# Performance work log

Hardware: AMD Instinct MI355X
Metric: run time of the kernel (lower is better)

## Reference

```python
import jax, jax.numpy as jnp
import numpy as np

D_MODEL = 1024
NUM_HEADS = 16
HEAD_DIM = D_MODEL // NUM_HEADS
BATCH, SEQ = 2, 2048


def setup_inputs() -> dict:
    key = jax.random.key(0)
    ks = jax.random.split(key, 11)
    s = 1.0 / np.sqrt(D_MODEL)
    inp = {
        "query": jax.random.normal(ks[0], (BATCH, SEQ, D_MODEL), jnp.float32),
        "key": jax.random.normal(ks[1], (BATCH, SEQ, D_MODEL), jnp.float32),
        "value": jax.random.normal(ks[2], (BATCH, SEQ, D_MODEL), jnp.float32),
        "q_w": jax.random.uniform(ks[3], (D_MODEL, D_MODEL), jnp.float32, -s, s),
        "q_b": jax.random.uniform(ks[4], (D_MODEL,), jnp.float32, -s, s),
        "k_w": jax.random.uniform(ks[5], (D_MODEL, D_MODEL), jnp.float32, -s, s),
        "k_b": jax.random.uniform(ks[6], (D_MODEL,), jnp.float32, -s, s),
        "v_w": jax.random.uniform(ks[7], (D_MODEL, D_MODEL), jnp.float32, -s, s),
        "v_b": jax.random.uniform(ks[8], (D_MODEL,), jnp.float32, -s, s),
        "o_w": jax.random.uniform(ks[9], (D_MODEL, D_MODEL), jnp.float32, -s, s),
        "o_b": jax.random.uniform(ks[10], (D_MODEL,), jnp.float32, -s, s),
    }
    return inp


def reference(query, key, value, q_w, q_b, k_w, k_b, v_w, v_b, o_w, o_b):
    B = query.shape[0]
    # linear projections (torch Linear: x @ W^T + b)
    q = query @ q_w.T + q_b
    k = key @ k_w.T + k_b
    v = value @ v_w.T + v_b
    # split heads: [B, S, D] -> [B, H, S, Hd]
    def split(x):
        return x.reshape(B, -1, NUM_HEADS, HEAD_DIM).transpose(0, 2, 1, 3)
    q, k, v = split(q), split(k), split(v)
    scores = jnp.einsum("bhqd,bhkd->bhqk", q, k) / np.sqrt(HEAD_DIM).astype(np.float32)
    attn = jax.nn.softmax(scores, axis=-1)
    out = jnp.einsum("bhqk,bhkd->bhqd", attn, v)  # [B,H,S,Hd]
    merged = out.transpose(0, 2, 1, 3).reshape(B, -1, D_MODEL)
    return merged @ o_w.T + o_b
```

## Files before the change

### kernel.cpp

```cpp
#include <hip/hip_runtime.h>
#include <hip/hip_bf16.h>

typedef unsigned short u16;
typedef unsigned int u32;
typedef __attribute__((ext_vector_type(8))) short short8;
typedef __attribute__((ext_vector_type(4))) short s16x4;
typedef __attribute__((ext_vector_type(4))) float f32x4;
typedef __attribute__((ext_vector_type(4))) u32 u32v4;

__device__ __forceinline__ u16 f2bf(float f) {
    u32 u = __float_as_uint(f);
    return (u16)((u + 0x7FFFu + ((u >> 16) & 1u)) >> 16);
}
__device__ __forceinline__ u32 pack2bf(float a, float b) {
    __hip_bfloat162 h = __float22bfloat162_rn(float2{a, b});
    return *reinterpret_cast<u32*>(&h);
}

#if __has_builtin(__builtin_amdgcn_exp2f)
#define EXP2(x) __builtin_amdgcn_exp2f(x)
#else
#define EXP2(x) exp2f(x)
#endif

__device__ __forceinline__ void gload16(const void* g, void* s) {
    __builtin_amdgcn_global_load_lds(
        (const __attribute__((address_space(1))) void*)g,
        (__attribute__((address_space(3))) void*)s, 16, 0, 0);
}

__global__ __launch_bounds__(256) void cast_all_kernel(
    const float* __restrict__ s0, const float* __restrict__ s1, const float* __restrict__ s2,
    const float* __restrict__ s3, const float* __restrict__ s4, const float* __restrict__ s5,
    const float* __restrict__ s6,
    u16* __restrict__ d0, u16* __restrict__ d1, u16* __restrict__ d2,
    u16* __restrict__ d3, u16* __restrict__ d4, u16* __restrict__ d5,
    u16* __restrict__ d6, int nBig, int nSmall)
{
    const int y = blockIdx.y;
    const float* s = y == 0 ? s0 : (y == 1 ? s1 : (y == 2 ? s2 : (y == 3 ? s3 : (y == 4 ? s4 : (y == 5 ? s5 : s6)))));
    u16* d = y == 0 ? d0 : (y == 1 ? d1 : (y == 2 ? d2 : (y == 3 ? d3 : (y == 4 ? d4 : (y == 5 ? d5 : d6)))));
    const int n = (y < 3) ? nBig : nSmall;
    int i = (blockIdx.x * 256 + threadIdx.x) * 4;
    const int stride = gridDim.x * 256 * 4;
    for (; i < n; i += stride) {
        float4 v = *(const float4*)(s + i);
        uint2 t;
        t.x = pack2bf(v.x, v.y);
        t.y = pack2bf(v.z, v.w);
        *(uint2*)(d + i) = t;
    }
}

__global__ __launch_bounds__(256) void qkv_gemm(
    const u16* __restrict__ Xq, const u16* __restrict__ Xk, const u16* __restrict__ Xv,
    const u16* __restrict__ Wq, const u16* __restrict__ Wk, const u16* __restrict__ Wv,
    const float* __restrict__ qb, const float* __restrict__ kb, const float* __restrict__ vb,
    u16* __restrict__ Qo, u16* __restrict__ Ko, u16* __restrict__ Vo)
{
    constexpr int N = 1024, K = 1024;
    __shared__ __align__(16) u16 Asm[2][4096];
    __shared__ __align__(16) u16 Bsm[2][4096];
    const int z = blockIdx.z;
    const u16* A = z == 0 ? Xq : (z == 1 ? Xk : Xv);
    const u16* W = z == 0 ? Wq : (z == 1 ? Wk : Wv);
    const float* bias = z == 0 ? qb : (z == 1 ? kb : vb);

    const int tid = threadIdx.x;
    const int wid = tid >> 6;
    const int lane = tid & 63;
    const int r15 = lane & 15, g = lane >> 4;
    const int fb = blockIdx.y * 8 + blockIdx.x;
    const int lsw = (fb & 7) * 32 + (fb >> 3);
    const int m0 = (lsw >> 3) * 128, n0 = (lsw & 7) * 128;
    const int wr = wid >> 1, wc = wid & 1;

    f32x4 acc[4][4];
#pragma unroll
    for (int i = 0; i < 4; ++i)
#pragma unroll
        for (int j = 0; j < 4; ++j) acc[i][j] = (f32x4){0.f, 0.f, 0.f, 0.f};

    const int idx0 = tid, idx1 = tid + 256;
    const size_t aoff0 = (size_t)(m0 + (idx0 >> 2)) * K + (idx0 & 3) * 8;
    const size_t aoff1 = (size_t)(m0 + (idx1 >> 2)) * K + (idx1 & 3) * 8;
    const size_t boff0 = (size_t)(n0 + (idx0 >> 2)) * K + (idx0 & 3) * 8;
    const size_t boff1 = (size_t)(n0 + (idx1 >> 2)) * K + (idx1 & 3) * 8;

    auto STAGE = [&](int buf, int kt) {
        gload16(A + aoff0 + kt, &Asm[buf][wid * 512]);
        gload16(A + aoff1 + kt, &Asm[buf][2048 + wid * 512]);
        gload16(W + boff0 + kt, &Bsm[buf][wid * 512]);
        gload16(W + boff1 + kt, &Bsm[buf][2048 + wid * 512]);
    };

    STAGE(0, 0);
    __syncthreads();
    for (int t = 0; t < 32; ++t) {
        const int buf = t & 1;
        if (t < 31) STAGE(buf ^ 1, (t + 1) * 32);
        short8 af[4], bfr[4];
#pragma unroll
        for (int i = 0; i < 4; ++i) {
            af[i]  = *(const short8*)(&Asm[buf][0] + (wr * 64 + i * 16 + r15) * 32 + g * 8);
            bfr[i] = *(const short8*)(&Bsm[buf][0] + (wc * 64 + i * 16 + r15) * 32 + g * 8);
        }
#pragma unroll
        for (int i = 0; i < 4; ++i)
#pragma unroll
            for (int j = 0; j < 4; ++j)
                acc[i][j] = __builtin_amdgcn_mfma_f32_16x16x32_bf16(af[i], bfr[j], acc[i][j], 0, 0, 0);
        __syncthreads();
    }

    const float scale = (z == 0) ? 0.125f * 1.4426950408889634f : 1.0f;
    u16* ob = z == 0 ? Qo : (z == 1 ? Ko : Vo);
#pragma unroll
    for (int i = 0; i < 4; ++i) {
        const int mbase = m0 + wr * 64 + i * 16 + g * 4;
#pragma unroll
        for (int j = 0; j < 4; ++j) {
            const int n = n0 + wc * 64 + j * 16 + r15;
            const float bb = bias[n];
            if (z < 2) {
#pragma unroll
                for (int r = 0; r < 4; ++r)
                    ob[(size_t)(mbase + r) * N + n] = f2bf((acc[i][j][r] + bb) * scale);
            } else {
                const int b_ = mbase >> 11, s_ = mbase & 2047;
                const int blk = (s_ >> 2) & 7;
                const int pb = ((blk & 3) << 1) | (blk >> 2);
                const int s_new = (s_ & ~31) | (pb << 2);
                s16x4 pk;
#pragma unroll
                for (int r = 0; r < 4; ++r) pk[r] = (short)f2bf(acc[i][j][r] + bb);
                *(s16x4*)(ob + ((size_t)b_ << 21) + (size_t)n * 2048 + s_new) = pk;
            }
        }
    }
}

__global__ __launch_bounds__(256) void o_gemm(
    const u16* __restrict__ A, const u16* __restrict__ W,
    const float* __restrict__ bias, float* __restrict__ outp)
{
    constexpr int N = 1024, K = 1024;
    __shared__ __align__(16) u16 Asm[2][4096];
    __shared__ __align__(16) u16 Bsm[2][4096];
    const int tid = threadIdx.x;
    const int wid = tid >> 6;
    const int lane = tid & 63;
    const int r15 = lane & 15, g = lane >> 4;
    const int fb = blockIdx.y * 8 + blockIdx.x;
    const int lsw = (fb & 7) * 32 + (fb >> 3);
    const int m0 = (lsw >> 3) * 128, n0 = (lsw & 7) * 128;
    const int wr = wid >> 1, wc = wid & 1;

    f32x4 acc[4][4];
#pragma unroll
    for (int i = 0; i < 4; ++i)
#pragma unroll
        for (int j = 0; j < 4; ++j) acc[i][j] = (f32x4){0.f, 0.f, 0.f, 0.f};

    const int idx0 = tid, idx1 = tid + 256;
    const size_t aoff0 = (size_t)(m0 + (idx0 >> 2)) * K + (idx0 & 3) * 8;
    const size_t aoff1 = (size_t)(m0 + (idx1 >> 2)) * K + (idx1 & 3) * 8;
    const size_t boff0 = (size_t)(n0 + (idx0 >> 2)) * K + (idx0 & 3) * 8;
    const size_t boff1 = (size_t)(n0 + (idx1 >> 2)) * K + (idx1 & 3) * 8;

    auto STAGE = [&](int buf, int kt) {
        gload16(A + aoff0 + kt, &Asm[buf][wid * 512]);
        gload16(A + aoff1 + kt, &Asm[buf][2048 + wid * 512]);
        gload16(W + boff0 + kt, &Bsm[buf][wid * 512]);
        gload16(W + boff1 + kt, &Bsm[buf][2048 + wid * 512]);
    };

    STAGE(0, 0);
    __syncthreads();
    for (int t = 0; t < 32; ++t) {
        const int buf = t & 1;
        if (t < 31) STAGE(buf ^ 1, (t + 1) * 32);
        short8 af[4], bfr[4];
#pragma unroll
        for (int i = 0; i < 4; ++i) {
            af[i]  = *(const short8*)(&Asm[buf][0] + (wr * 64 + i * 16 + r15) * 32 + g * 8);
            bfr[i] = *(const short8*)(&Bsm[buf][0] + (wc * 64 + i * 16 + r15) * 32 + g * 8);
        }
#pragma unroll
        for (int i = 0; i < 4; ++i)
#pragma unroll
            for (int j = 0; j < 4; ++j)
                acc[i][j] = __builtin_amdgcn_mfma_f32_16x16x32_bf16(af[i], bfr[j], acc[i][j], 0, 0, 0);
        __syncthreads();
    }

#pragma unroll
    for (int i = 0; i < 4; ++i) {
        const int mbase = m0 + wr * 64 + i * 16 + g * 4;
#pragma unroll
        for (int j = 0; j < 4; ++j) {
            const int n = n0 + wc * 64 + j * 16 + r15;
            const float bb = bias[n];
#pragma unroll
            for (int r = 0; r < 4; ++r)
                outp[(size_t)(mbase + r) * N + n] = acc[i][j][r] + bb;
        }
    }
}

__global__ __launch_bounds__(256) void attn_kernel(
    const u16* __restrict__ Q, const u16* __restrict__ Kb,
    const u16* __restrict__ Vt, u16* __restrict__ Mo)
{
    __shared__ __align__(16) u16 Ksm[2][4096];
    __shared__ __align__(16) u16 Vsm[2][4096];
    const int tid = threadIdx.x;
    const int wid = tid >> 6, lane = tid & 63;
    const int r15 = lane & 15, g = lane >> 4;
    const int bid = blockIdx.x;
    const int l = (bid & 7) * 64 + (bid >> 3);
    const int bh = l >> 4;
    const int b = bh >> 4, h = bh & 15;
    const int q0 = (l & 15) * 128 + wid * 32;

    const u16* Qbase = Q + ((size_t)b * 2048 + q0) * 1024 + h * 64;
    short8 qf[2][2];
#pragma unroll
    for (int qt = 0; qt < 2; ++qt)
#pragma unroll
        for (int f = 0; f < 2; ++f)
            qf[qt][f] = *(const short8*)(Qbase + (size_t)(qt * 16 + r15) * 1024 + f * 32 + g * 8);

    const int p0 = tid, p1 = tid + 256;
    const int row0 = p0 >> 3, slot0 = (p0 & 7) ^ (row0 & 7);
    const int row1 = p1 >> 3, slot1 = (p1 & 7) ^ (row1 & 7);
    const u16* Ks0 = Kb + ((size_t)b * 2048 + row0) * 1024 + h * 64 + slot0 * 8;
    const u16* Ks1 = Kb + ((size_t)b * 2048 + row1) * 1024 + h * 64 + slot1 * 8;
    const u16* Vs0 = Vt + ((size_t)b << 21) + (size_t)(h * 64 + row0) * 2048 + slot0 * 8;
    const u16* Vs1 = Vt + ((size_t)b << 21) + (size_t)(h * 64 + row1) * 2048 + slot1 * 8;

    f32x4 acc[2][4];
#pragma unroll
    for (int qt = 0; qt < 2; ++qt)
#pragma unroll
        for (int d4 = 0; d4 < 4; ++d4) acc[qt][d4] = (f32x4){0.f, 0.f, 0.f, 0.f};
    float lsum[2] = {0.f, 0.f};

    auto STAGE = [&](int buf, int k0) {
        gload16(Ks0 + (size_t)k0 * 1024, &Ksm[buf][wid * 512]);
        gload16(Ks1 + (size_t)k0 * 1024, &Ksm[buf][2048 + wid * 512]);
        gload16(Vs0 + k0, &Vsm[buf][wid * 512]);
        gload16(Vs1 + k0, &Vsm[buf][2048 + wid * 512]);
    };

    STAGE(0, 0);
    __syncthreads();

    const int sA = r15 & 7;
    for (int t = 0; t < 32; ++t) {
        const int buf = t & 1;
        if (t < 31) STAGE(buf ^ 1, (t + 1) * 64);

        const u16* Kp = &Ksm[buf][0];
        const u16* Vp = &Vsm[buf][0];
        short8 kf[4][2];
#pragma unroll
        for (int kt = 0; kt < 4; ++kt)
#pragma unroll
            for (int f = 0; f < 2; ++f)
                kf[kt][f] = *(const short8*)(Kp + (kt * 16 + r15) * 64 + (((f * 4 + g) ^ sA) * 8));

        f32x4 st[2][4];
#pragma unroll
        for (int qt = 0; qt < 2; ++qt)
#pragma unroll
            for (int kt = 0; kt < 4; ++kt) {
                f32x4 zz = (f32x4){0.f, 0.f, 0.f, 0.f};
                zz = __builtin_amdgcn_mfma_f32_16x16x32_bf16(kf[kt][0], qf[qt][0], zz, 0, 0, 0);
                zz = __builtin_amdgcn_mfma_f32_16x16x32_bf16(kf[kt][1], qf[qt][1], zz, 0, 0, 0);
                st[qt][kt] = zz;
            }

        u32 pk[2][8];
#pragma unroll
        for (int qt = 0; qt < 2; ++qt) {
            float s = 0.f;
#pragma unroll
            for (int kt = 0; kt < 4; ++kt) {
                float e0 = EXP2(st[qt][kt][0]);
                float e1 = EXP2(st[qt][kt][1]);
                float e2 = EXP2(st[qt][kt][2]);
                float e3 = EXP2(st[qt][kt][3]);
                s += (e0 + e1) + (e2 + e3);
                pk[qt][kt * 2]     = pack2bf(e0, e1);
                pk[qt][kt * 2 + 1] = pack2bf(e2, e3);
            }
            lsum[qt] += s;
        }

#pragma unroll
        for (int d4 = 0; d4 < 4; ++d4) {
#pragma unroll
            for (int kk = 0; kk < 2; ++kk) {
                short8 vf = *(const short8*)(Vp + (d4 * 16 + r15) * 64 + (((kk * 4 + g) ^ sA) * 8));
                u32v4 b0 = {pk[0][kk * 4], pk[0][kk * 4 + 1], pk[0][kk * 4 + 2], pk[0][kk * 4 + 3]};
                u32v4 b1 = {pk[1][kk * 4], pk[1][kk * 4 + 1], pk[1][kk * 4 + 2], pk[1][kk * 4 + 3]};
                acc[0][d4] = __builtin_amdgcn_mfma_f32_16x16x32_bf16(vf, __builtin_bit_cast(short8, b0), acc[0][d4], 0, 0, 0);
                acc[1][d4] = __builtin_amdgcn_mfma_f32_16x16x32_bf16(vf, __builtin_bit_cast(short8, b1), acc[1][d4], 0, 0, 0);
            }
        }
        __syncthreads();
    }

#pragma unroll
    for (int qt = 0; qt < 2; ++qt) {
        float ls = lsum[qt];
        ls += __shfl_xor(ls, 16, 64);
        ls += __shfl_xor(ls, 32, 64);
        const float inv = 1.f / ls;
        const size_t orow = ((size_t)b * 2048 + q0 + qt * 16 + r15) * 1024 + h * 64;
#pragma unroll
        for (int d4 = 0; d4 < 4; ++d4) {
            uint2 o;
            o.x = pack2bf(acc[qt][d4][0] * inv, acc[qt][d4][1] * inv);
            o.y = pack2bf(acc[qt][d4][2] * inv, acc[qt][d4][3] * inv);
            *(uint2*)(Mo + orow + d4 * 16 + g * 4) = o;
        }
    }
}

extern "C" void kernel_launch(void* const* d_in, const int* in_sizes, int n_in,
                              void* d_out, int out_size, void* d_ws, size_t ws_size,
                              hipStream_t stream) {
    (void)in_sizes; (void)n_in; (void)out_size; (void)ws_size;
    const float* query = (const float*)d_in[0];
    const float* key   = (const float*)d_in[1];
    const float* value = (const float*)d_in[2];
    const float* q_w = (const float*)d_in[3];
    const float* q_b = (const float*)d_in[4];
    const float* k_w = (const float*)d_in[5];
    const float* k_b = (const float*)d_in[6];
    const float* v_w = (const float*)d_in[7];
    const float* v_b = (const float*)d_in[8];
    const float* o_w = (const float*)d_in[9];
    const float* o_b = (const float*)d_in[10];

    const size_t NE = (size_t)4096 * 1024;
    const size_t MW = (size_t)1024 * 1024;
    u16* w = (u16*)d_ws;
    u16* Xq = w;
    u16* Xk = Xq + NE;
    u16* Xv = Xk + NE;
    u16* Wq = Xv + NE;
    u16* Wk = Wq + MW;
    u16* Wv = Wk + MW;
    u16* Wo = Wv + MW;
    u16* Qb = Wo + MW;
    u16* Kb = Qb + NE;
    u16* Vt = Kb + NE;
    u16* Mo = Vt + NE;

    cast_all_kernel<<<dim3(2048, 7), 256, 0, stream>>>(
        query, key, value, q_w, k_w, v_w, o_w,
        Xq, Xk, Xv, Wq, Wk, Wv, Wo, (int)NE, (int)MW);
    qkv_gemm<<<dim3(8, 32, 3), 256, 0, stream>>>(
        Xq, Xk, Xv, Wq, Wk, Wv, q_b, k_b, v_b, Qb, Kb, Vt);
    attn_kernel<<<dim3(512), 256, 0, stream>>>(Qb, Kb, Vt, Mo);
    o_gemm<<<dim3(8, 32), 256, 0, stream>>>(Mo, Wo, o_b, (float*)d_out);
}
```

Measured before the change: 142.7 us.

## Fuse activation bf16 cast into QKV GEMM and compute softmax row sums via MFMA

```diff
diff --git a/kernel.cpp b/kernel.cpp
--- a/kernel.cpp
+++ b/kernel.cpp
@@ -16,12 +16,11 @@
     __hip_bfloat162 h = __float22bfloat162_rn(float2{a, b});
     return *reinterpret_cast<u32*>(&h);
 }
-
-#if __has_builtin(__builtin_amdgcn_exp2f)
-#define EXP2(x) __builtin_amdgcn_exp2f(x)
-#else
-#define EXP2(x) exp2f(x)
-#endif
+__device__ __forceinline__ float exp2hw(float x) {
+    float r;
+    asm("v_exp_f32 %0, %1" : "=v"(r) : "v"(x));
+    return r;
+}
 
 __device__ __forceinline__ void gload16(const void* g, void* s) {
     __builtin_amdgcn_global_load_lds(
@@ -29,21 +28,17 @@
         (__attribute__((address_space(3))) void*)s, 16, 0, 0);
 }
 
-__global__ __launch_bounds__(256) void cast_all_kernel(
-    const float* __restrict__ s0, const float* __restrict__ s1, const float* __restrict__ s2,
-    const float* __restrict__ s3, const float* __restrict__ s4, const float* __restrict__ s5,
-    const float* __restrict__ s6,
+__global__ __launch_bounds__(256) void cast_w_kernel(
+    const float* __restrict__ s0, const float* __restrict__ s1,
+    const float* __restrict__ s2, const float* __restrict__ s3,
     u16* __restrict__ d0, u16* __restrict__ d1, u16* __restrict__ d2,
-    u16* __restrict__ d3, u16* __restrict__ d4, u16* __restrict__ d5,
-    u16* __restrict__ d6, int nBig, int nSmall)
+    u16* __restrict__ d3, int n)
 {
     const int y = blockIdx.y;
-    const float* s = y == 0 ? s0 : (y == 1 ? s1 : (y == 2 ? s2 : (y == 3 ? s3 : (y == 4 ? s4 : (y == 5 ? s5 : s6)))));
-    u16* d = y == 0 ? d0 : (y == 1 ? d1 : (y == 2 ? d2 : (y == 3 ? d3 : (y == 4 ? d4 : (y == 5 ? d5 : d6)))));
-    const int n = (y < 3) ? nBig : nSmall;
+    const float* s = y == 0 ? s0 : (y == 1 ? s1 : (y == 2 ? s2 : s3));
+    u16* d = y == 0 ? d0 : (y == 1 ? d1 : (y == 2 ? d2 : d3));
     int i = (blockIdx.x * 256 + threadIdx.x) * 4;
-    const int stride = gridDim.x * 256 * 4;
-    for (; i < n; i += stride) {
+    if (i < n) {
         float4 v = *(const float4*)(s + i);
         uint2 t;
         t.x = pack2bf(v.x, v.y);
@@ -53,7 +48,7 @@
 }
 
 __global__ __launch_bounds__(256) void qkv_gemm(
-    const u16* __restrict__ Xq, const u16* __restrict__ Xk, const u16* __restrict__ Xv,
+    const float* __restrict__ Xq, const float* __restrict__ Xk, const float* __restrict__ Xv,
     const u16* __restrict__ Wq, const u16* __restrict__ Wk, const u16* __restrict__ Wv,
     const float* __restrict__ qb, const float* __restrict__ kb, const float* __restrict__ vb,
     u16* __restrict__ Qo, u16* __restrict__ Ko, u16* __restrict__ Vo)
@@ -62,7 +57,7 @@
     __shared__ __align__(16) u16 Asm[2][4096];
     __shared__ __align__(16) u16 Bsm[2][4096];
     const int z = blockIdx.z;
-    const u16* A = z == 0 ? Xq : (z == 1 ? Xk : Xv);
+    const float* Afp = z == 0 ? Xq : (z == 1 ? Xk : Xv);
     const u16* W = z == 0 ? Wq : (z == 1 ? Wk : Wv);
     const float* bias = z == 0 ? qb : (z == 1 ? kb : vb);
 
@@ -81,35 +76,58 @@
 #pragma unroll
         for (int j = 0; j < 4; ++j) acc[i][j] = (f32x4){0.f, 0.f, 0.f, 0.f};
 
+    const float* Abase = Afp + (size_t)(m0 + (tid >> 3)) * 1024 + (tid & 7) * 4;
+    const int wboff = (tid >> 3) * 32 + (tid & 7) * 4;
     const int idx0 = tid, idx1 = tid + 256;
-    const size_t aoff0 = (size_t)(m0 + (idx0 >> 2)) * K + (idx0 & 3) * 8;
-    const size_t aoff1 = (size_t)(m0 + (idx1 >> 2)) * K + (idx1 & 3) * 8;
     const size_t boff0 = (size_t)(n0 + (idx0 >> 2)) * K + (idx0 & 3) * 8;
     const size_t boff1 = (size_t)(n0 + (idx1 >> 2)) * K + (idx1 & 3) * 8;
-
-    auto STAGE = [&](int buf, int kt) {
-        gload16(A + aoff0 + kt, &Asm[buf][wid * 512]);
-        gload16(A + aoff1 + kt, &Asm[buf][2048 + wid * 512]);
-        gload16(W + boff0 + kt, &Bsm[buf][wid * 512]);
-        gload16(W + boff1 + kt, &Bsm[buf][2048 + wid * 512]);
-    };
-
-    STAGE(0, 0);
+    const u16* abase = &Asm[0][0] + (wr * 64 + r15) * 32 + g * 8;
+    const u16* bbase = &Bsm[0][0] + (wc * 64 + r15) * 32 + g * 8;
+
+    float4 L[4];
+#pragma unroll
+    for (int c = 0; c < 4; ++c) L[c] = *(const float4*)(Abase + c * 32768);
+    gload16(W + boff0, &Bsm[0][wid * 512]);
+    gload16(W + boff1, &Bsm[0][2048 + wid * 512]);
+    {
+        u16* wb = &Asm[0][0] + wboff;
+#pragma unroll
+        for (int c = 0; c < 4; ++c) {
+            uint2 t{pack2bf(L[c].x, L[c].y), pack2bf(L[c].z, L[c].w)};
+            *(uint2*)(wb + c * 1024) = t;
+        }
+    }
     __syncthreads();
+
+#pragma unroll 2
     for (int t = 0; t < 32; ++t) {
         const int buf = t & 1;
-        if (t < 31) STAGE(buf ^ 1, (t + 1) * 32);
+        if (t < 31) {
+            const int kt = (t + 1) * 32;
+#pragma unroll
+            for (int c = 0; c < 4; ++c) L[c] = *(const float4*)(Abase + c * 32768 + kt);
+            gload16(W + boff0 + kt, &Bsm[buf ^ 1][wid * 512]);
+            gload16(W + boff1 + kt, &Bsm[buf ^ 1][2048 + wid * 512]);
+        }
         short8 af[4], bfr[4];
 #pragma unroll
         for (int i = 0; i < 4; ++i) {
-            af[i]  = *(const short8*)(&Asm[buf][0] + (wr * 64 + i * 16 + r15) * 32 + g * 8);
-            bfr[i] = *(const short8*)(&Bsm[buf][0] + (wc * 64 + i * 16 + r15) * 32 + g * 8);
+            af[i]  = *(const short8*)(abase + buf * 4096 + i * 512);
+            bfr[i] = *(const short8*)(bbase + buf * 4096 + i * 512);
         }
 #pragma unroll
         for (int i = 0; i < 4; ++i)
 #pragma unroll
             for (int j = 0; j < 4; ++j)
                 acc[i][j] = __builtin_amdgcn_mfma_f32_16x16x32_bf16(af[i], bfr[j], acc[i][j], 0, 0, 0);
+        if (t < 31) {
+            u16* wb = &Asm[buf ^ 1][0] + wboff;
+#pragma unroll
+            for (int c = 0; c < 4; ++c) {
+                uint2 tt{pack2bf(L[c].x, L[c].y), pack2bf(L[c].z, L[c].w)};
+                *(uint2*)(wb + c * 1024) = tt;
+            }
+        }
         __syncthreads();
     }
 
@@ -167,24 +185,30 @@
     const size_t aoff1 = (size_t)(m0 + (idx1 >> 2)) * K + (idx1 & 3) * 8;
     const size_t boff0 = (size_t)(n0 + (idx0 >> 2)) * K + (idx0 & 3) * 8;
     const size_t boff1 = (size_t)(n0 + (idx1 >> 2)) * K + (idx1 & 3) * 8;
-
-    auto STAGE = [&](int buf, int kt) {
-        gload16(A + aoff0 + kt, &Asm[buf][wid * 512]);
-        gload16(A + aoff1 + kt, &Asm[buf][2048 + wid * 512]);
-        gload16(W + boff0 + kt, &Bsm[buf][wid * 512]);
-        gload16(W + boff1 + kt, &Bsm[buf][2048 + wid * 512]);
-    };
-
-    STAGE(0, 0);
+    const u16* abase = &Asm[0][0] + (wr * 64 + r15) * 32 + g * 8;
+    const u16* bbase = &Bsm[0][0] + (wc * 64 + r15) * 32 + g * 8;
+
+    gload16(A + aoff0, &Asm[0][wid * 512]);
+    gload16(A + aoff1, &Asm[0][2048 + wid * 512]);
+    gload16(W + boff0, &Bsm[0][wid * 512]);
+    gload16(W + boff1, &Bsm[0][2048 + wid * 512]);
     __syncthreads();
+
+#pragma unroll 2
     for (int t = 0; t < 32; ++t) {
         const int buf = t & 1;
-        if (t < 31) STAGE(buf ^ 1, (t + 1) * 32);
+        if (t < 31) {
+            const int kt = (t + 1) * 32;
+            gload16(A + aoff0 + kt, &Asm[buf ^ 1][wid * 512]);
+            gload16(A + aoff1 + kt, &Asm[buf ^ 1][2048 + wid * 512]);
+            gload16(W + boff0 + kt, &Bsm[buf ^ 1][wid * 512]);
+            gload16(W + boff1 + kt, &Bsm[buf ^ 1][2048 + wid * 512]);
+        }
         short8 af[4], bfr[4];
 #pragma unroll
         for (int i = 0; i < 4; ++i) {
-            af[i]  = *(const short8*)(&Asm[buf][0] + (wr * 64 + i * 16 + r15) * 32 + g * 8);
-            bfr[i] = *(const short8*)(&Bsm[buf][0] + (wc * 64 + i * 16 + r15) * 32 + g * 8);
+            af[i]  = *(const short8*)(abase + buf * 4096 + i * 512);
+            bfr[i] = *(const short8*)(bbase + buf * 4096 + i * 512);
         }
 #pragma unroll
         for (int i = 0; i < 4; ++i)
@@ -232,43 +256,53 @@
             qf[qt][f] = *(const short8*)(Qbase + (size_t)(qt * 16 + r15) * 1024 + f * 32 + g * 8);
 
     const int p0 = tid, p1 = tid + 256;
-    const int row0 = p0 >> 3, slot0 = (p0 & 7) ^ (row0 & 7);
-    const int row1 = p1 >> 3, slot1 = (p1 & 7) ^ (row1 & 7);
-    const u16* Ks0 = Kb + ((size_t)b * 2048 + row0) * 1024 + h * 64 + slot0 * 8;
-    const u16* Ks1 = Kb + ((size_t)b * 2048 + row1) * 1024 + h * 64 + slot1 * 8;
-    const u16* Vs0 = Vt + ((size_t)b << 21) + (size_t)(h * 64 + row0) * 2048 + slot0 * 8;
-    const u16* Vs1 = Vt + ((size_t)b << 21) + (size_t)(h * 64 + row1) * 2048 + slot1 * 8;
+    const int row0 = p0 >> 3, slot0s = (p0 & 7) ^ (row0 & 7);
+    const int row1 = p1 >> 3, slot1s = (p1 & 7) ^ (row1 & 7);
+    const u16* Ks0 = Kb + ((size_t)b * 2048 + row0) * 1024 + h * 64 + slot0s * 8;
+    const u16* Ks1 = Kb + ((size_t)b * 2048 + row1) * 1024 + h * 64 + slot1s * 8;
+    const u16* Vs0 = Vt + ((size_t)b << 21) + (size_t)(h * 64 + row0) * 2048 + slot0s * 8;
+    const u16* Vs1 = Vt + ((size_t)b << 21) + (size_t)(h * 64 + row1) * 2048 + slot1s * 8;
+
+    const int sA = r15 & 7;
+    const int sl0 = (g ^ sA) * 8;
+    const int sl1 = sl0 ^ 32;
+    const u16* kb0 = &Ksm[0][0] + r15 * 64 + sl0;
+    const u16* kb1 = &Ksm[0][0] + r15 * 64 + sl1;
+    const u16* vb0 = &Vsm[0][0] + r15 * 64 + sl0;
+    const u16* vb1 = &Vsm[0][0] + r15 * 64 + sl1;
 
     f32x4 acc[2][4];
 #pragma unroll
     for (int qt = 0; qt < 2; ++qt)
 #pragma unroll
         for (int d4 = 0; d4 < 4; ++d4) acc[qt][d4] = (f32x4){0.f, 0.f, 0.f, 0.f};
-    float lsum[2] = {0.f, 0.f};
-
-    auto STAGE = [&](int buf, int k0) {
-        gload16(Ks0 + (size_t)k0 * 1024, &Ksm[buf][wid * 512]);
-        gload16(Ks1 + (size_t)k0 * 1024, &Ksm[buf][2048 + wid * 512]);
-        gload16(Vs0 + k0, &Vsm[buf][wid * 512]);
-        gload16(Vs1 + k0, &Vsm[buf][2048 + wid * 512]);
-    };
-
-    STAGE(0, 0);
+    f32x4 accl[2] = {(f32x4){0.f, 0.f, 0.f, 0.f}, (f32x4){0.f, 0.f, 0.f, 0.f}};
+    const short8 vone = {0x3F80, 0x3F80, 0x3F80, 0x3F80, 0x3F80, 0x3F80, 0x3F80, 0x3F80};
+
+    gload16(Ks0, &Ksm[0][wid * 512]);
+    gload16(Ks1, &Ksm[0][2048 + wid * 512]);
+    gload16(Vs0, &Vsm[0][wid * 512]);
+    gload16(Vs1, &Vsm[0][2048 + wid * 512]);
+    Ks0 += 65536; Ks1 += 65536; Vs0 += 64; Vs1 += 64;
     __syncthreads();
 
-    const int sA = r15 & 7;
+#pragma unroll 2
     for (int t = 0; t < 32; ++t) {
         const int buf = t & 1;
-        if (t < 31) STAGE(buf ^ 1, (t + 1) * 64);
-
-        const u16* Kp = &Ksm[buf][0];
-        const u16* Vp = &Vsm[buf][0];
+        if (t < 31) {
+            gload16(Ks0, &Ksm[buf ^ 1][wid * 512]);
+            gload16(Ks1, &Ksm[buf ^ 1][2048 + wid * 512]);
+            gload16(Vs0, &Vsm[buf ^ 1][wid * 512]);
+            gload16(Vs1, &Vsm[buf ^ 1][2048 + wid * 512]);
+            Ks0 += 65536; Ks1 += 65536; Vs0 += 64; Vs1 += 64;
+        }
+
         short8 kf[4][2];
 #pragma unroll
-        for (int kt = 0; kt < 4; ++kt)
-#pragma unroll
-            for (int f = 0; f < 2; ++f)
-                kf[kt][f] = *(const short8*)(Kp + (kt * 16 + r15) * 64 + (((f * 4 + g) ^ sA) * 8));
+        for (int kt = 0; kt < 4; ++kt) {
+            kf[kt][0] = *(const short8*)(kb0 + buf * 4096 + kt * 1024);
+            kf[kt][1] = *(const short8*)(kb1 + buf * 4096 + kt * 1024);
+        }
 
         f32x4 st[2][4];
 #pragma unroll
@@ -281,43 +315,42 @@
                 st[qt][kt] = zz;
             }
 
-        u32 pk[2][8];
+        u32v4 pA[2], pB[2];
 #pragma unroll
         for (int qt = 0; qt < 2; ++qt) {
-            float s = 0.f;
 #pragma unroll
             for (int kt = 0; kt < 4; ++kt) {
-                float e0 = EXP2(st[qt][kt][0]);
-                float e1 = EXP2(st[qt][kt][1]);
-                float e2 = EXP2(st[qt][kt][2]);
-                float e3 = EXP2(st[qt][kt][3]);
-                s += (e0 + e1) + (e2 + e3);
-                pk[qt][kt * 2]     = pack2bf(e0, e1);
-                pk[qt][kt * 2 + 1] = pack2bf(e2, e3);
+                float e0 = exp2hw(st[qt][kt][0]);
+                float e1 = exp2hw(st[qt][kt][1]);
+                float e2 = exp2hw(st[qt][kt][2]);
+                float e3 = exp2hw(st[qt][kt][3]);
+                u32 lo = pack2bf(e0, e1);
+                u32 hi = pack2bf(e2, e3);
+                if (kt < 2) { pA[qt][kt * 2] = lo; pA[qt][kt * 2 + 1] = hi; }
+                else        { pB[qt][(kt - 2) * 2] = lo; pB[qt][(kt - 2) * 2 + 1] = hi; }
             }
-            lsum[qt] += s;
-        }
+        }
+
+        accl[0] = __builtin_amdgcn_mfma_f32_16x16x32_bf16(vone, __builtin_bit_cast(short8, pA[0]), accl[0], 0, 0, 0);
+        accl[0] = __builtin_amdgcn_mfma_f32_16x16x32_bf16(vone, __builtin_bit_cast(short8, pB[0]), accl[0], 0, 0, 0);
+        accl[1] = __builtin_amdgcn_mfma_f32_16x16x32_bf16(vone, __builtin_bit_cast(short8, pA[1]), accl[1], 0, 0, 0);
+        accl[1] = __builtin_amdgcn_mfma_f32_16x16x32_bf16(vone, __builtin_bit_cast(short8, pB[1]), accl[1], 0, 0, 0);
 
 #pragma unroll
         for (int d4 = 0; d4 < 4; ++d4) {
-#pragma unroll
-            for (int kk = 0; kk < 2; ++kk) {
-                short8 vf = *(const short8*)(Vp + (d4 * 16 + r15) * 64 + (((kk * 4 + g) ^ sA) * 8));
-                u32v4 b0 = {pk[0][kk * 4], pk[0][kk * 4 + 1], pk[0][kk * 4 + 2], pk[0][kk * 4 + 3]};
-                u32v4 b1 = {pk[1][kk * 4], pk[1][kk * 4 + 1], pk[1][kk * 4 + 2], pk[1][kk * 4 + 3]};
-                acc[0][d4] = __builtin_amdgcn_mfma_f32_16x16x32_bf16(vf, __builtin_bit_cast(short8, b0), acc[0][d4], 0, 0, 0);
-                acc[1][d4] = __builtin_amdgcn_mfma_f32_16x16x32_bf16(vf, __builtin_bit_cast(short8, b1), acc[1][d4], 0, 0, 0);
-            }
+            short8 vf0 = *(const short8*)(vb0 + buf * 4096 + d4 * 1024);
+            short8 vf1 = *(const short8*)(vb1 + buf * 4096 + d4 * 1024);
+            acc[0][d4] = __builtin_amdgcn_mfma_f32_16x16x32_bf16(vf0, __builtin_bit_cast(short8, pA[0]), acc[0][d4], 0, 0, 0);
+            acc[0][d4] = __builtin_amdgcn_mfma_f32_16x16x32_bf16(vf1, __builtin_bit_cast(short8, pB[0]), acc[0][d4], 0, 0, 0);
+            acc[1][d4] = __builtin_amdgcn_mfma_f32_16x16x32_bf16(vf0, __builtin_bit_cast(short8, pA[1]), acc[1][d4], 0, 0, 0);
+            acc[1][d4] = __builtin_amdgcn_mfma_f32_16x16x32_bf16(vf1, __builtin_bit_cast(short8, pB[1]), acc[1][d4], 0, 0, 0);
         }
         __syncthreads();
     }
 
 #pragma unroll
     for (int qt = 0; qt < 2; ++qt) {
-        float ls = lsum[qt];
-        ls += __shfl_xor(ls, 16, 64);
-        ls += __shfl_xor(ls, 32, 64);
-        const float inv = 1.f / ls;
+        const float inv = 1.f / accl[qt][0];
         const size_t orow = ((size_t)b * 2048 + q0 + qt * 16 + r15) * 1024 + h * 64;
 #pragma unroll
         for (int d4 = 0; d4 < 4; ++d4) {
@@ -348,10 +381,7 @@
     const size_t NE = (size_t)4096 * 1024;
     const size_t MW = (size_t)1024 * 1024;
     u16* w = (u16*)d_ws;
-    u16* Xq = w;
-    u16* Xk = Xq + NE;
-    u16* Xv = Xk + NE;
-    u16* Wq = Xv + NE;
+    u16* Wq = w;
     u16* Wk = Wq + MW;
     u16* Wv = Wk + MW;
     u16* Wo = Wv + MW;
@@ -360,11 +390,10 @@
     u16* Vt = Kb + NE;
     u16* Mo = Vt + NE;
 
-    cast_all_kernel<<<dim3(2048, 7), 256, 0, stream>>>(
-        query, key, value, q_w, k_w, v_w, o_w,
-        Xq, Xk, Xv, Wq, Wk, Wv, Wo, (int)NE, (int)MW);
+    cast_w_kernel<<<dim3(1024, 4), 256, 0, stream>>>(
+        q_w, k_w, v_w, o_w, Wq, Wk, Wv, Wo, (int)MW);
     qkv_gemm<<<dim3(8, 32, 3), 256, 0, stream>>>(
-        Xq, Xk, Xv, Wq, Wk, Wv, q_b, k_b, v_b, Qb, Kb, Vt);
+        query, key, value, Wq, Wk, Wv, q_b, k_b, v_b, Qb, Kb, Vt);
     attn_kernel<<<dim3(512), 256, 0, stream>>>(Qb, Kb, Vt, Mo);
     o_gemm<<<dim3(8, 32), 256, 0, stream>>>(Mo, Wo, o_b, (float*)d_out);
 }
```

Measured after the change: 139.8 us. -2.0%, faster.

## Halve attention query tile per block and compute row sums via MFMA

Applied to the files above, without the earlier changes.

```diff
diff --git a/kernel.cpp b/kernel.cpp
--- a/kernel.cpp
+++ b/kernel.cpp
@@ -16,12 +16,11 @@
     __hip_bfloat162 h = __float22bfloat162_rn(float2{a, b});
     return *reinterpret_cast<u32*>(&h);
 }
-
-#if __has_builtin(__builtin_amdgcn_exp2f)
-#define EXP2(x) __builtin_amdgcn_exp2f(x)
-#else
-#define EXP2(x) exp2f(x)
-#endif
+__device__ __forceinline__ float exp2hw(float x) {
+    float r;
+    asm("v_exp_f32 %0, %1" : "=v"(r) : "v"(x));
+    return r;
+}
 
 __device__ __forceinline__ void gload16(const void* g, void* s) {
     __builtin_amdgcn_global_load_lds(
@@ -218,114 +217,106 @@
     const int wid = tid >> 6, lane = tid & 63;
     const int r15 = lane & 15, g = lane >> 4;
     const int bid = blockIdx.x;
-    const int l = (bid & 7) * 64 + (bid >> 3);
-    const int bh = l >> 4;
+    const int l = (bid & 7) * 128 + (bid >> 3);
+    const int bh = l >> 5;
     const int b = bh >> 4, h = bh & 15;
-    const int q0 = (l & 15) * 128 + wid * 32;
-
-    const u16* Qbase = Q + ((size_t)b * 2048 + q0) * 1024 + h * 64;
-    short8 qf[2][2];
-#pragma unroll
-    for (int qt = 0; qt < 2; ++qt)
-#pragma unroll
-        for (int f = 0; f < 2; ++f)
-            qf[qt][f] = *(const short8*)(Qbase + (size_t)(qt * 16 + r15) * 1024 + f * 32 + g * 8);
+    const int q0 = (l & 31) * 64 + wid * 16;
+
+    const u16* Qrow = Q + ((size_t)b * 2048 + q0 + r15) * 1024 + h * 64;
+    short8 qf[2];
+    qf[0] = *(const short8*)(Qrow + g * 8);
+    qf[1] = *(const short8*)(Qrow + 32 + g * 8);
 
     const int p0 = tid, p1 = tid + 256;
-    const int row0 = p0 >> 3, slot0 = (p0 & 7) ^ (row0 & 7);
-    const int row1 = p1 >> 3, slot1 = (p1 & 7) ^ (row1 & 7);
-    const u16* Ks0 = Kb + ((size_t)b * 2048 + row0) * 1024 + h * 64 + slot0 * 8;
-    const u16* Ks1 = Kb + ((size_t)b * 2048 + row1) * 1024 + h * 64 + slot1 * 8;
-    const u16* Vs0 = Vt + ((size_t)b << 21) + (size_t)(h * 64 + row0) * 2048 + slot0 * 8;
-    const u16* Vs1 = Vt + ((size_t)b << 21) + (size_t)(h * 64 + row1) * 2048 + slot1 * 8;
-
-    f32x4 acc[2][4];
-#pragma unroll
-    for (int qt = 0; qt < 2; ++qt)
-#pragma unroll
-        for (int d4 = 0; d4 < 4; ++d4) acc[qt][d4] = (f32x4){0.f, 0.f, 0.f, 0.f};
-    float lsum[2] = {0.f, 0.f};
-
-    auto STAGE = [&](int buf, int k0) {
-        gload16(Ks0 + (size_t)k0 * 1024, &Ksm[buf][wid * 512]);
-        gload16(Ks1 + (size_t)k0 * 1024, &Ksm[buf][2048 + wid * 512]);
-        gload16(Vs0 + k0, &Vsm[buf][wid * 512]);
-        gload16(Vs1 + k0, &Vsm[buf][2048 + wid * 512]);
-    };
-
-    STAGE(0, 0);
+    const int row0 = p0 >> 3, slot0s = (p0 & 7) ^ (row0 & 7);
+    const int row1 = p1 >> 3, slot1s = (p1 & 7) ^ (row1 & 7);
+    const u16* Ks0 = Kb + ((size_t)b * 2048 + row0) * 1024 + h * 64 + slot0s * 8;
+    const u16* Ks1 = Kb + ((size_t)b * 2048 + row1) * 1024 + h * 64 + slot1s * 8;
+    const u16* Vs0 = Vt + ((size_t)b << 21) + (size_t)(h * 64 + row0) * 2048 + slot0s * 8;
+    const u16* Vs1 = Vt + ((size_t)b << 21) + (size_t)(h * 64 + row1) * 2048 + slot1s * 8;
+
+    const int sA = r15 & 7;
+    const int sl0 = (g ^ sA) * 8;
+    const int sl1 = sl0 ^ 32;
+    const u16* kb0 = &Ksm[0][0] + r15 * 64 + sl0;
+    const u16* kb1 = &Ksm[0][0] + r15 * 64 + sl1;
+    const u16* vb0 = &Vsm[0][0] + r15 * 64 + sl0;
+    const u16* vb1 = &Vsm[0][0] + r15 * 64 + sl1;
+
+    f32x4 acc[4];
+#pragma unroll
+    for (int d4 = 0; d4 < 4; ++d4) acc[d4] = (f32x4){0.f, 0.f, 0.f, 0.f};
+    f32x4 accl = (f32x4){0.f, 0.f, 0.f, 0.f};
+    const short8 vone = {0x3F80, 0x3F80, 0x3F80, 0x3F80, 0x3F80, 0x3F80, 0x3F80, 0x3F80};
+
+    gload16(Ks0, &Ksm[0][wid * 512]);
+    gload16(Ks1, &Ksm[0][2048 + wid * 512]);
+    gload16(Vs0, &Vsm[0][wid * 512]);
+    gload16(Vs1, &Vsm[0][2048 + wid * 512]);
+    Ks0 += 65536; Ks1 += 65536; Vs0 += 64; Vs1 += 64;
     __syncthreads();
 
-    const int sA = r15 & 7;
+#pragma unroll 2
     for (int t = 0; t < 32; ++t) {
         const int buf = t & 1;
-        if (t < 31) STAGE(buf ^ 1, (t + 1) * 64);
-
-        const u16* Kp = &Ksm[buf][0];
-        const u16* Vp = &Vsm[buf][0];
+        if (t < 31) {
+            gload16(Ks0, &Ksm[buf ^ 1][wid * 512]);
+            gload16(Ks1, &Ksm[buf ^ 1][2048 + wid * 512]);
+            gload16(Vs0, &Vsm[buf ^ 1][wid * 512]);
+            gload16(Vs1, &Vsm[buf ^ 1][2048 + wid * 512]);
+            Ks0 += 65536; Ks1 += 65536; Vs0 += 64; Vs1 += 64;
+        }
+
         short8 kf[4][2];
 #pragma unroll
-        for (int kt = 0; kt < 4; ++kt)
-#pragma unroll
-            for (int f = 0; f < 2; ++f)
-                kf[kt][f] = *(const short8*)(Kp + (kt * 16 + r15) * 64 + (((f * 4 + g) ^ sA) * 8));
-
-        f32x4 st[2][4];
-#pragma unroll
-        for (int qt = 0; qt < 2; ++qt)
-#pragma unroll
-            for (int kt = 0; kt < 4; ++kt) {
-                f32x4 zz = (f32x4){0.f, 0.f, 0.f, 0.f};
-                zz = __builtin_amdgcn_mfma_f32_16x16x32_bf16(kf[kt][0], qf[qt][0], zz, 0, 0, 0);
-                zz = __builtin_amdgcn_mfma_f32_16x16x32_bf16(kf[kt][1], qf[qt][1], zz, 0, 0, 0);
-                st[qt][kt] = zz;
-            }
-
-        u32 pk[2][8];
-#pragma unroll
-        for (int qt = 0; qt < 2; ++qt) {
-            float s = 0.f;
-#pragma unroll
-            for (int kt = 0; kt < 4; ++kt) {
-                float e0 = EXP2(st[qt][kt][0]);
-                float e1 = EXP2(st[qt][kt][1]);
-                float e2 = EXP2(st[qt][kt][2]);
-                float e3 = EXP2(st[qt][kt][3]);
-                s += (e0 + e1) + (e2 + e3);
-                pk[qt][kt * 2]     = pack2bf(e0, e1);
-                pk[qt][kt * 2 + 1] = pack2bf(e2, e3);
-            }
-            lsum[qt] += s;
-        }
+        for (int kt = 0; kt < 4; ++kt) {
+            kf[kt][0] = *(const short8*)(kb0 + buf * 4096 + kt * 1024);
+            kf[kt][1] = *(const short8*)(kb1 + buf * 4096 + kt * 1024);
+        }
+
+        f32x4 st[4];
+#pragma unroll
+        for (int kt = 0; kt < 4; ++kt) {
+            f32x4 zz = (f32x4){0.f, 0.f, 0.f, 0.f};
+            zz = __builtin_amdgcn_mfma_f32_16x16x32_bf16(kf[kt][0], qf[0], zz, 0, 0, 0);
+            zz = __builtin_amdgcn_mfma_f32_16x16x32_bf16(kf[kt][1], qf[1], zz, 0, 0, 0);
+            st[kt] = zz;
+        }
+
+        u32v4 pA, pB;
+#pragma unroll
+        for (int kt = 0; kt < 4; ++kt) {
+            float e0 = exp2hw(st[kt][0]);
+            float e1 = exp2hw(st[kt][1]);
+            float e2 = exp2hw(st[kt][2]);
+            float e3 = exp2hw(st[kt][3]);
+            u32 lo = pack2bf(e0, e1);
+            u32 hi = pack2bf(e2, e3);
+            if (kt < 2) { pA[kt * 2] = lo; pA[kt * 2 + 1] = hi; }
+            else        { pB[(kt - 2) * 2] = lo; pB[(kt - 2) * 2 + 1] = hi; }
+        }
+
+        accl = __builtin_amdgcn_mfma_f32_16x16x32_bf16(vone, __builtin_bit_cast(short8, pA), accl, 0, 0, 0);
+        accl = __builtin_amdgcn_mfma_f32_16x16x32_bf16(vone, __builtin_bit_cast(short8, pB), accl, 0, 0, 0);
 
 #pragma unroll
         for (int d4 = 0; d4 < 4; ++d4) {
-#pragma unroll
-            for (int kk = 0; kk < 2; ++kk) {
-                short8 vf = *(const short8*)(Vp + (d4 * 16 + r15) * 64 + (((kk * 4 + g) ^ sA) * 8));
-                u32v4 b0 = {pk[0][kk * 4], pk[0][kk * 4 + 1], pk[0][kk * 4 + 2], pk[0][kk * 4 + 3]};
-                u32v4 b1 = {pk[1][kk * 4], pk[1][kk * 4 + 1], pk[1][kk * 4 + 2], pk[1][kk * 4 + 3]};
-                acc[0][d4] = __builtin_amdgcn_mfma_f32_16x16x32_bf16(vf, __builtin_bit_cast(short8, b0), acc[0][d4], 0, 0, 0);
-                acc[1][d4] = __builtin_amdgcn_mfma_f32_16x16x32_bf16(vf, __builtin_bit_cast(short8, b1), acc[1][d4], 0, 0, 0);
-            }
+            short8 vf0 = *(const short8*)(vb0 + buf * 4096 + d4 * 1024);
+            short8 vf1 = *(const short8*)(vb1 + buf * 4096 + d4 * 1024);
+            acc[d4] = __builtin_amdgcn_mfma_f32_16x16x32_bf16(vf0, __builtin_bit_cast(short8, pA), acc[d4], 0, 0, 0);
+            acc[d4] = __builtin_amdgcn_mfma_f32_16x16x32_bf16(vf1, __builtin_bit_cast(short8, pB), acc[d4], 0, 0, 0);
         }
         __syncthreads();
     }
 
-#pragma unroll
-    for (int qt = 0; qt < 2; ++qt) {
-        float ls = lsum[qt];
-        ls += __shfl_xor(ls, 16, 64);
-        ls += __shfl_xor(ls, 32, 64);
-        const float inv = 1.f / ls;
-        const size_t orow = ((size_t)b * 2048 + q0 + qt * 16 + r15) * 1024 + h * 64;
-#pragma unroll
-        for (int d4 = 0; d4 < 4; ++d4) {
-            uint2 o;
-            o.x = pack2bf(acc[qt][d4][0] * inv, acc[qt][d4][1] * inv);
-            o.y = pack2bf(acc[qt][d4][2] * inv, acc[qt][d4][3] * inv);
-            *(uint2*)(Mo + orow + d4 * 16 + g * 4) = o;
-        }
+    const float inv = 1.f / accl[0];
+    const size_t orow = ((size_t)b * 2048 + q0 + r15) * 1024 + h * 64;
+#pragma unroll
+    for (int d4 = 0; d4 < 4; ++d4) {
+        uint2 o;
+        o.x = pack2bf(acc[d4][0] * inv, acc[d4][1] * inv);
+        o.y = pack2bf(acc[d4][2] * inv, acc[d4][3] * inv);
+        *(uint2*)(Mo + orow + d4 * 16 + g * 4) = o;
     }
 }
 
@@ -365,6 +356,6 @@
         Xq, Xk, Xv, Wq, Wk, Wv, Wo, (int)NE, (int)MW);
     qkv_gemm<<<dim3(8, 32, 3), 256, 0, stream>>>(
         Xq, Xk, Xv, Wq, Wk, Wv, q_b, k_b, v_b, Qb, Kb, Vt);
-    attn_kernel<<<dim3(512), 256, 0, stream>>>(Qb, Kb, Vt, Mo);
+    attn_kernel<<<dim3(1024), 256, 0, stream>>>(Qb, Kb, Vt, Mo);
     o_gemm<<<dim3(8, 32), 256, 0, stream>>>(Mo, Wo, o_b, (float*)d_out);
 }
```

Result: faster. 133.8 us (-6.2%).

## Load K/V fragments directly from global in single-wave attention blocks, MFMA row sums

Applied to the files above, without the earlier changes.

```diff
diff --git a/kernel.cpp b/kernel.cpp
--- a/kernel.cpp
+++ b/kernel.cpp
@@ -16,7 +16,6 @@
     __hip_bfloat162 h = __float22bfloat162_rn(float2{a, b});
     return *reinterpret_cast<u32*>(&h);
 }
-
 #if __has_builtin(__builtin_amdgcn_exp2f)
 #define EXP2(x) __builtin_amdgcn_exp2f(x)
 #else
@@ -208,20 +207,17 @@
     }
 }
 
-__global__ __launch_bounds__(256) void attn_kernel(
+__global__ __launch_bounds__(64) void attn_kernel(
     const u16* __restrict__ Q, const u16* __restrict__ Kb,
     const u16* __restrict__ Vt, u16* __restrict__ Mo)
 {
-    __shared__ __align__(16) u16 Ksm[2][4096];
-    __shared__ __align__(16) u16 Vsm[2][4096];
-    const int tid = threadIdx.x;
-    const int wid = tid >> 6, lane = tid & 63;
+    const int lane = threadIdx.x;
     const int r15 = lane & 15, g = lane >> 4;
     const int bid = blockIdx.x;
-    const int l = (bid & 7) * 64 + (bid >> 3);
-    const int bh = l >> 4;
+    const int l = (bid & 7) * 256 + (bid >> 3);
+    const int bh = l >> 6;
     const int b = bh >> 4, h = bh & 15;
-    const int q0 = (l & 15) * 128 + wid * 32;
+    const int q0 = (l & 63) * 32;
 
     const u16* Qbase = Q + ((size_t)b * 2048 + q0) * 1024 + h * 64;
     short8 qf[2][2];
@@ -231,44 +227,31 @@
         for (int f = 0; f < 2; ++f)
             qf[qt][f] = *(const short8*)(Qbase + (size_t)(qt * 16 + r15) * 1024 + f * 32 + g * 8);
 
-    const int p0 = tid, p1 = tid + 256;
-    const int row0 = p0 >> 3, slot0 = (p0 & 7) ^ (row0 & 7);
-    const int row1 = p1 >> 3, slot1 = (p1 & 7) ^ (row1 & 7);
-    const u16* Ks0 = Kb + ((size_t)b * 2048 + row0) * 1024 + h * 64 + slot0 * 8;
-    const u16* Ks1 = Kb + ((size_t)b * 2048 + row1) * 1024 + h * 64 + slot1 * 8;
-    const u16* Vs0 = Vt + ((size_t)b << 21) + (size_t)(h * 64 + row0) * 2048 + slot0 * 8;
-    const u16* Vs1 = Vt + ((size_t)b << 21) + (size_t)(h * 64 + row1) * 2048 + slot1 * 8;
+    const u16* Kp = Kb + ((size_t)b * 2048 + r15) * 1024 + h * 64 + g * 8;
+    const u16* Vp = Vt + ((size_t)b << 21) + (size_t)(h * 64 + r15) * 2048 + g * 8;
 
     f32x4 acc[2][4];
 #pragma unroll
     for (int qt = 0; qt < 2; ++qt)
 #pragma unroll
         for (int d4 = 0; d4 < 4; ++d4) acc[qt][d4] = (f32x4){0.f, 0.f, 0.f, 0.f};
-    float lsum[2] = {0.f, 0.f};
-
-    auto STAGE = [&](int buf, int k0) {
-        gload16(Ks0 + (size_t)k0 * 1024, &Ksm[buf][wid * 512]);
-        gload16(Ks1 + (size_t)k0 * 1024, &Ksm[buf][2048 + wid * 512]);
-        gload16(Vs0 + k0, &Vsm[buf][wid * 512]);
-        gload16(Vs1 + k0, &Vsm[buf][2048 + wid * 512]);
-    };
-
-    STAGE(0, 0);
-    __syncthreads();
-
-    const int sA = r15 & 7;
+    f32x4 accl[2] = {(f32x4){0.f, 0.f, 0.f, 0.f}, (f32x4){0.f, 0.f, 0.f, 0.f}};
+    const short8 vone = {0x3F80, 0x3F80, 0x3F80, 0x3F80, 0x3F80, 0x3F80, 0x3F80, 0x3F80};
+
     for (int t = 0; t < 32; ++t) {
-        const int buf = t & 1;
-        if (t < 31) STAGE(buf ^ 1, (t + 1) * 64);
-
-        const u16* Kp = &Ksm[buf][0];
-        const u16* Vp = &Vsm[buf][0];
-        short8 kf[4][2];
-#pragma unroll
-        for (int kt = 0; kt < 4; ++kt)
-#pragma unroll
-            for (int f = 0; f < 2; ++f)
-                kf[kt][f] = *(const short8*)(Kp + (kt * 16 + r15) * 64 + (((f * 4 + g) ^ sA) * 8));
+        const u16* Kt = Kp + (size_t)t * 65536;
+        const u16* Vc = Vp + t * 64;
+        short8 kf[4][2], vf[4][2];
+#pragma unroll
+        for (int kt = 0; kt < 4; ++kt) {
+            kf[kt][0] = *(const short8*)(Kt + kt * 16384);
+            kf[kt][1] = *(const short8*)(Kt + kt * 16384 + 32);
+        }
+#pragma unroll
+        for (int d4 = 0; d4 < 4; ++d4) {
+            vf[d4][0] = *(const short8*)(Vc + d4 * 32768);
+            vf[d4][1] = *(const short8*)(Vc + d4 * 32768 + 32);
+        }
 
         f32x4 st[2][4];
 #pragma unroll
@@ -281,43 +264,39 @@
                 st[qt][kt] = zz;
             }
 
-        u32 pk[2][8];
+        u32v4 pA[2], pB[2];
 #pragma unroll
         for (int qt = 0; qt < 2; ++qt) {
-            float s = 0.f;
 #pragma unroll
             for (int kt = 0; kt < 4; ++kt) {
                 float e0 = EXP2(st[qt][kt][0]);
                 float e1 = EXP2(st[qt][kt][1]);
                 float e2 = EXP2(st[qt][kt][2]);
                 float e3 = EXP2(st[qt][kt][3]);
-                s += (e0 + e1) + (e2 + e3);
-                pk[qt][kt * 2]     = pack2bf(e0, e1);
-                pk[qt][kt * 2 + 1] = pack2bf(e2, e3);
+                u32 lo = pack2bf(e0, e1);
+                u32 hi = pack2bf(e2, e3);
+                if (kt < 2) { pA[qt][kt * 2] = lo; pA[qt][kt * 2 + 1] = hi; }
+                else        { pB[qt][(kt - 2) * 2] = lo; pB[qt][(kt - 2) * 2 + 1] = hi; }
             }
-            lsum[qt] += s;
-        }
+        }
+
+        accl[0] = __builtin_amdgcn_mfma_f32_16x16x32_bf16(vone, __builtin_bit_cast(short8, pA[0]), accl[0], 0, 0, 0);
+        accl[0] = __builtin_amdgcn_mfma_f32_16x16x32_bf16(vone, __builtin_bit_cast(short8, pB[0]), accl[0], 0, 0, 0);
+        accl[1] = __builtin_amdgcn_mfma_f32_16x16x32_bf16(vone, __builtin_bit_cast(short8, pA[1]), accl[1], 0, 0, 0);
+        accl[1] = __builtin_amdgcn_mfma_f32_16x16x32_bf16(vone, __builtin_bit_cast(short8, pB[1]), accl[1], 0, 0, 0);
 
 #pragma unroll
         for (int d4 = 0; d4 < 4; ++d4) {
-#pragma unroll
-            for (int kk = 0; kk < 2; ++kk) {
-                short8 vf = *(const short8*)(Vp + (d4 * 16 + r15) * 64 + (((kk * 4 + g) ^ sA) * 8));
-                u32v4 b0 = {pk[0][kk * 4], pk[0][kk * 4 + 1], pk[0][kk * 4 + 2], pk[0][kk * 4 + 3]};
-                u32v4 b1 = {pk[1][kk * 4], pk[1][kk * 4 + 1], pk[1][kk * 4 + 2], pk[1][kk * 4 + 3]};
-                acc[0][d4] = __builtin_amdgcn_mfma_f32_16x16x32_bf16(vf, __builtin_bit_cast(short8, b0), acc[0][d4], 0, 0, 0);
-                acc[1][d4] = __builtin_amdgcn_mfma_f32_16x16x32_bf16(vf, __builtin_bit_cast(short8, b1), acc[1][d4], 0, 0, 0);
-            }
-        }
-        __syncthreads();
+            acc[0][d4] = __builtin_amdgcn_mfma_f32_16x16x32_bf16(vf[d4][0], __builtin_bit_cast(short8, pA[0]), acc[0][d4], 0, 0, 0);
+            acc[0][d4] = __builtin_amdgcn_mfma_f32_16x16x32_bf16(vf[d4][1], __builtin_bit_cast(short8, pB[0]), acc[0][d4], 0, 0, 0);
+            acc[1][d4] = __builtin_amdgcn_mfma_f32_16x16x32_bf16(vf[d4][0], __builtin_bit_cast(short8, pA[1]), acc[1][d4], 0, 0, 0);
+            acc[1][d4] = __builtin_amdgcn_mfma_f32_16x16x32_bf16(vf[d4][1], __builtin_bit_cast(short8, pB[1]), acc[1][d4], 0, 0, 0);
+        }
     }
 
 #pragma unroll
     for (int qt = 0; qt < 2; ++qt) {
-        float ls = lsum[qt];
-        ls += __shfl_xor(ls, 16, 64);
-        ls += __shfl_xor(ls, 32, 64);
-        const float inv = 1.f / ls;
+        const float inv = 1.f / accl[qt][0];
         const size_t orow = ((size_t)b * 2048 + q0 + qt * 16 + r15) * 1024 + h * 64;
 #pragma unroll
         for (int d4 = 0; d4 < 4; ++d4) {
@@ -365,6 +344,6 @@
         Xq, Xk, Xv, Wq, Wk, Wv, Wo, (int)NE, (int)MW);
     qkv_gemm<<<dim3(8, 32, 3), 256, 0, stream>>>(
         Xq, Xk, Xv, Wq, Wk, Wv, q_b, k_b, v_b, Qb, Kb, Vt);
-    attn_kernel<<<dim3(512), 256, 0, stream>>>(Qb, Kb, Vt, Mo);
+    attn_kernel<<<dim3(2048), 64, 0, stream>>>(Qb, Kb, Vt, Mo);
     o_gemm<<<dim3(8, 32), 256, 0, stream>>>(Mo, Wo, o_b, (float*)d_out);
 }
```

After: 202.1 us. +41.6%, slower.
